# Kernel tuning notes

Measured on AMD Instinct MI355X. Metric: run time of the kernel, lower is better.

## Reference

```python
import jax, jax.numpy as jnp
import numpy as np

N = 24000      # total nodes (8000 per node type)
IN_DIM = 128
OUT_DIM = 128
H = 8          # heads
DK = 16        # out_dim // n_heads
T = 3          # node types (hard-coded in edge_attention)
R = 34         # relations (etypes 0..33 per the etype->ntype rules)
EPR = 10000    # edges per relation (DGL applies edge fn per etype)


def _rel_node_types(num_rel):
    # src/dst node type per relation, transcribed from edge_attention
    src_nt = np.array([0 if r <= 9 else (1 if r <= 21 else 2) for r in range(num_rel)], np.int32)
    def _dnt(r):
        if r <= 2 or 10 <= r <= 13 or 22 <= r <= 24:
            return 0
        if 3 <= r <= 6 or 14 <= r <= 17 or 25 <= r <= 28:
            return 1
        return 2
    dst_nt = np.array([_dnt(r) for r in range(num_rel)], np.int32)
    return src_nt, dst_nt

SRC_NT, DST_NT = _rel_node_types(R)


def setup_inputs() -> dict:
    rng = np.random.default_rng(0)
    Nt = N // T  # nodes of type t live in [t*Nt, (t+1)*Nt)
    src = np.stack([rng.integers(SRC_NT[r] * Nt, (SRC_NT[r] + 1) * Nt, EPR) for r in range(R)]).astype(np.int32)
    dst = np.stack([rng.integers(DST_NT[r] * Nt, (DST_NT[r] + 1) * Nt, EPR) for r in range(R)]).astype(np.int32)
    ks = jax.random.split(jax.random.key(0), 10)
    lin = 1.0 / np.sqrt(IN_DIM)
    return {
        'x': jax.random.normal(ks[0], (N, IN_DIM), jnp.float32),
        'src': jnp.asarray(src),
        'dst': jnp.asarray(dst),
        'Wk': jax.random.normal(ks[1], (T, IN_DIM, OUT_DIM), jnp.float32) * lin,
        'bk': jnp.zeros((T, OUT_DIM), jnp.float32),
        'Wq': jax.random.normal(ks[2], (T, IN_DIM, OUT_DIM), jnp.float32) * lin,
        'bq': jnp.zeros((T, OUT_DIM), jnp.float32),
        'Wv': jax.random.normal(ks[3], (T, IN_DIM, OUT_DIM), jnp.float32) * lin,
        'bv': jnp.zeros((T, OUT_DIM), jnp.float32),
        'Wa': jax.random.normal(ks[4], (T, OUT_DIM, OUT_DIM), jnp.float32) * lin,
        'ba': jnp.zeros((T, OUT_DIM), jnp.float32),
        'rel_att': jax.random.normal(ks[5], (R, H, DK, DK), jnp.float32) / np.sqrt(DK),
        'rel_msg': jax.random.normal(ks[6], (R, H, DK, DK), jnp.float32) / np.sqrt(DK),
        'rel_pri': jnp.ones((R, H), jnp.float32),
        'nta': jnp.ones((T,), jnp.float32),
        'nta1': jnp.ones((T,), jnp.float32),
        'skip': jnp.ones((T,), jnp.float32),
        'weight': jnp.ones((1,), jnp.float32),
        'attn_w': jax.random.normal(ks[7], (2 * DK,), jnp.float32) * 0.1,
    }


def reference(x, src, dst, Wk, bk, Wq, bq, Wv, bv, Wa, ba, rel_att, rel_msg, rel_pri, nta, nta1, skip, weight, attn_w):
    ntype = jnp.repeat(jnp.arange(T), N // T)  # node type per node id
    ridx = jnp.arange(N)

    def typed_lin(h, W, b):
        # per-node-type Linear: compute all T projections, select by node type
        return (jnp.einsum('ni,tio->tno', h, W) + b[:, None, :])[ntype, ridx]

    k = typed_lin(x, Wk, bk).reshape(N, H, DK)
    q = typed_lin(x, Wq, bq).reshape(N, H, DK)
    v = typed_lin(x, Wv, bv).reshape(N, H, DK)

    k_src = k[src]                                   # [R, Epr, H, DK]
    q_dst = q[dst]                                   # [R, Epr, H, DK]
    key_t = jnp.einsum('rehd,rhdf->rehf', k_src, rel_att)
    a = (q_dst * key_t).sum(-1) * rel_pri[:, None, :] / np.sqrt(DK)   # [R, Epr, H]
    val = jnp.einsum('rehd,rhdf->rehf', v[src], rel_msg)              # [R, Epr, H, DK]

    # GAT-style concat attention: attn_fc(cat(att_dst*q, att_src*k)) split into two dots
    wq, wk = attn_w[:DK], attn_w[DK:]
    na = jax.nn.leaky_relu(nta1[DST_NT][:, None, None] * (q_dst @ wq)
                           + nta[SRC_NT][:, None, None] * (k_src @ wk))  # [R, Epr, H]

    beta = jax.nn.sigmoid(weight[0])
    s = (a + beta * na).reshape(R * EPR, H)

    # per-(relation, dst-node) segment softmax (DGL mailbox softmax per etype)
    seg = (jnp.arange(R)[:, None] * N + dst).reshape(-1)
    m = jax.ops.segment_max(s, seg, num_segments=R * N)
    e = jnp.exp(s - m[seg])
    den = jax.ops.segment_sum(e, seg, num_segments=R * N)
    att = e / den[seg]

    vf = val.reshape(R * EPR, H, DK)
    h = jax.ops.segment_sum(att[:, :, None] * vf, seg, num_segments=R * N).reshape(R, N, OUT_DIM)

    # cross_reducer='mean': average over relations that delivered messages to a node
    cnt = jax.ops.segment_sum(jnp.ones((R * EPR,), x.dtype), seg, num_segments=R * N).reshape(R, N)
    nrel = jnp.maximum((cnt > 0).astype(x.dtype).sum(0), 1.0)
    t = h.sum(0) / nrel[:, None]                      # [N, OUT_DIM]

    trans = (jnp.einsum('no,top->tnp', t, Wa) + ba[:, None, :])[ntype, ridx]
    alpha = jax.nn.sigmoid(skip)[ntype][:, None]
    return trans * alpha + x * (1.0 - alpha)
```

## Files before the change

kernel.cpp:

```cpp
#include <hip/hip_runtime.h>

#define NN   24000
#define NTP  8000
#define HH   8
#define DKK  16
#define RR   34
#define EPRN 10000
#define NE   (RR*EPRN)
#define NB   (RR*NTP)
#define CAP  16
#define NSCAT ((NE+255)/256)
#define LOG2E 1.4426950408889634f

typedef short short8 __attribute__((ext_vector_type(8)));
typedef _Float16 half8 __attribute__((ext_vector_type(8)));
typedef float f32x4  __attribute__((ext_vector_type(4)));
typedef _Float16 h2v __attribute__((ext_vector_type(2)));

#if defined(__has_builtin)
# if __has_builtin(__builtin_amdgcn_fdot2)
#  define USE_FDOT2 1
# endif
#endif
#ifndef USE_FDOT2
# define USE_FDOT2 0
#endif

__device__ __forceinline__ int src_nt(int r){ return r<=9?0:(r<=21?1:2); }
__device__ __forceinline__ int dst_nt(int r){
    if (r<=2)  return 0;
    if (r<=6)  return 1;
    if (r<=9)  return 2;
    if (r<=13) return 0;
    if (r<=17) return 1;
    if (r<=21) return 2;
    if (r<=24) return 0;
    if (r<=28) return 1;
    return 2;
}

__device__ __forceinline__ unsigned short bf16rne(float a){
    unsigned int u = __float_as_uint(a);
    u += 0x7fffu + ((u >> 16) & 1u);
    return (unsigned short)(u >> 16);
}
__device__ __forceinline__ unsigned int bf2pack(float a, float b){
    unsigned int ua = __float_as_uint(a);
    unsigned int ub = __float_as_uint(b);
    ua += 0x7fffu + ((ua >> 16) & 1u);
    ub += 0x7fffu + ((ub >> 16) & 1u);
    return (ua >> 16) | (ub & 0xffff0000u);
}
__device__ __forceinline__ unsigned short f16bits(float a){
    _Float16 h = (_Float16)a;
    return __builtin_bit_cast(unsigned short, h);
}

__global__ __launch_bounds__(256) void prep_kernel(
    const float* __restrict__ Wk, const float* __restrict__ Wq,
    const float* __restrict__ Wv, const float* __restrict__ Wa,
    const float* __restrict__ rel_att, const float* __restrict__ rel_msg,
    int* __restrict__ counts, unsigned short* __restrict__ wfrag,
    unsigned short* __restrict__ fragAtt, unsigned short* __restrict__ fragMsg)
{
    const int gid = blockIdx.x * 256 + threadIdx.x;
    if (gid < NB) counts[gid] = 0;
    const int wv   = threadIdx.x >> 6;
    const int lane = threadIdx.x & 63;
    const int m16  = lane & 15, quad = lane >> 4;
    if (blockIdx.x < 96) {
        const int tile = blockIdx.x * 4 + wv;
        const float* W;
        int s, n;
        if (tile < 288) {
            s = tile & 3;
            n = (tile >> 2) & 7;
            const int mat = (tile >> 5) % 3;
            const int tau = tile / 96;
            W = (mat == 0 ? Wk : (mat == 1 ? Wq : Wv)) + (size_t)tau * 16384;
        } else {
            const int t2 = tile - 288;
            s = t2 & 3;
            n = (t2 >> 2) & 7;
            const int tau = t2 >> 5;
            W = Wa + (size_t)tau * 16384;
        }
        const int k0  = s * 32 + quad * 8;
        const int col = n * 16 + m16;
        unsigned short* dstp = wfrag + (size_t)tile * 512 + lane * 8;
        #pragma unroll
        for (int i = 0; i < 8; i++)
            dstp[i] = bf16rne(W[(size_t)(k0 + i) * 128 + col]);
    } else if (blockIdx.x < 164) {
        const int rh = (blockIdx.x - 96) * 4 + wv;
        half8 v;
        #pragma unroll
        for (int i = 0; i < 8; i++) v[i] = (_Float16)0.f;
        if (quad < 2) {
            const float* p = rel_att + ((size_t)rh << 8) + m16 * 16 + quad * 8;
            #pragma unroll
            for (int i = 0; i < 8; i++) v[i] = (_Float16)p[i];
        }
        *(half8*)(fragAtt + ((size_t)rh << 9) + lane * 8) = v;
    } else if (blockIdx.x < 232) {
        const int rh = (blockIdx.x - 164) * 4 + wv;
        half8 v;
        #pragma unroll
        for (int i = 0; i < 8; i++) v[i] = (_Float16)0.f;
        if (quad < 2) {
            const float* Mp = rel_msg + ((size_t)rh << 8);
            #pragma unroll
            for (int i = 0; i < 8; i++) v[i] = (_Float16)Mp[(quad * 8 + i) * 16 + m16];
        }
        *(half8*)(fragMsg + ((size_t)rh << 9) + lane * 8) = v;
    }
}

__global__ __launch_bounds__(256) void work1(
    const float* __restrict__ x,
    const float* __restrict__ bk, const float* __restrict__ bq,
    const float* __restrict__ bv,
    const unsigned short* __restrict__ wfrag,
    const int* __restrict__ src, const int* __restrict__ dst,
    int* __restrict__ counts, int* __restrict__ esrc16,
    float* __restrict__ qo, unsigned short* __restrict__ kvh,
    const float* __restrict__ attn_w,
    float* __restrict__ qwqA, float* __restrict__ kwkA)
{
    __shared__ float qs[4][16][132];
    __shared__ unsigned short ksh[4][16][264];

    if (blockIdx.x >= 375) {
        int e = (blockIdx.x - 375) * 256 + threadIdx.x;
        if (e < NE) {
            int r = e / EPRN;
            int b = r * NTP + (dst[e] - dst_nt(r) * NTP);
            int pos = atomicAdd(&counts[b], 1);
            if (pos < CAP) esrc16[(size_t)b * CAP + pos] = src[e];
        }
        return;
    }

    const int rb   = blockIdx.x * 64;
    const int tau  = rb / NTP;
    const int w    = threadIdx.x >> 6;
    const int lane = threadIdx.x & 63;
    const int m    = lane & 15;
    const int quad = lane >> 4;

    short8 af[4];
    {
        const float* xrow = x + (size_t)(rb + w * 16 + m) * 128;
        #pragma unroll
        for (int s = 0; s < 4; s++) {
            float4 f0 = *(const float4*)(xrow + s * 32 + quad * 8);
            float4 f1 = *(const float4*)(xrow + s * 32 + quad * 8 + 4);
            union { unsigned int u[4]; short8 v; } pk;
            pk.u[0] = bf2pack(f0.x, f0.y); pk.u[1] = bf2pack(f0.z, f0.w);
            pk.u[2] = bf2pack(f1.x, f1.y); pk.u[3] = bf2pack(f1.z, f1.w);
            af[s] = pk.v;
        }
    }

    #pragma unroll
    for (int mat = 0; mat < 3; mat++) {
        const float* bias = (mat == 0 ? bk : (mat == 1 ? bq : bv)) + tau * 128;
        #pragma unroll
        for (int n = 0; n < 8; n++) {
            float bb = bias[n * 16 + m];
            f32x4 acc = {bb, bb, bb, bb};
            #pragma unroll
            for (int s = 0; s < 4; s++) {
                const int tile = ((tau * 3 + mat) * 8 + n) * 4 + s;
                short8 bf = *(const short8*)(wfrag + (size_t)tile * 512 + lane * 8);
                acc = __builtin_amdgcn_mfma_f32_16x16x32_bf16(af[s], bf, acc, 0, 0, 0);
            }
            if (mat == 1) {
                #pragma unroll
                for (int i = 0; i < 4; i++) qs[w][quad * 4 + i][n * 16 + m] = acc[i];
            } else {
                const int off = n * 32 + (mat == 0 ? 0 : 16) + m;
                #pragma unroll
                for (int i = 0; i < 4; i++) ksh[w][quad * 4 + i][off] = f16bits(acc[i]);
            }
        }
        if (mat == 1) {
            __syncthreads();
            #pragma unroll
            for (int j = 0; j < 8; j++) {
                const int id = lane + 64 * j;
                const int row = id >> 5, c4 = id & 31;
                float4 v = *(const float4*)(&qs[w][row][c4 * 4]);
                *(float4*)(qo + (size_t)(rb + w * 16 + row) * 128 + c4 * 4) = v;
            }
        }
    }
    __syncthreads();
    #pragma unroll
    for (int j = 0; j < 8; j++) {
        const int id = lane + 64 * j;
        const int row = id >> 5, c8 = id & 31;
        uint4 u = *(const uint4*)(&ksh[w][row][c8 * 8]);
        *(uint4*)(kvh + (size_t)(rb + w * 16 + row) * 256 + c8 * 8) = u;
    }
    #pragma unroll
    for (int rep = 0; rep < 2; rep++) {
        const int idx = threadIdx.x + rep * 256;
        const int row = idx >> 3, hh = idx & 7;
        const float* qrow = &qs[row >> 4][row & 15][hh * 16];
        const unsigned short* krow = &ksh[row >> 4][row & 15][hh * 32];
        float sq = 0.f, sk = 0.f;
        #pragma unroll
        for (int f = 0; f < 16; f++) {
            sq += qrow[f] * attn_w[f];
            sk += (float)__builtin_bit_cast(_Float16, krow[f]) * attn_w[16 + f];
        }
        qwqA[(size_t)(rb + row) * 8 + hh] = sq;
        kwkA[(size_t)(rb + row) * 8 + hh] = sk;
    }
}

__global__ __launch_bounds__(256) void edge_fused(
    const float* __restrict__ q, const unsigned short* __restrict__ kvh,
    const int* __restrict__ esrc16, const int* __restrict__ counts,
    const unsigned short* __restrict__ fragAtt,
    const unsigned short* __restrict__ fragMsg,
    const float* __restrict__ rel_pri,
    const float* __restrict__ nta, const float* __restrict__ nta1,
    const float* __restrict__ weightp,
    const float* __restrict__ qwqA, const float* __restrict__ kwkA,
    unsigned short* __restrict__ t_bf)
{
    __shared__ float tl[4][64][18];

    const int tid  = threadIdx.x;
    const int w    = tid >> 6;
    const int lane = tid & 63;
    const int h    = __builtin_amdgcn_readfirstlane((tid >> 6) + 4 * blockIdx.y);
    const int base = blockIdx.x * 64;
    const int dn   = base + lane;
    const int dtau = __builtin_amdgcn_readfirstlane(dn / NTP);
    const int dl   = dn - dtau * NTP;
    const int m16  = lane & 15, quad = lane >> 4;

    half8 qf[4];
    #pragma unroll
    for (int g = 0; g < 4; g++) {
        half8 t;
        #pragma unroll
        for (int i = 0; i < 8; i++) t[i] = (_Float16)0.f;
        if (quad < 2) {
            const float* qp = q + (size_t)(base + g * 16 + m16) * 128 + h * 16 + quad * 8;
            #pragma unroll
            for (int i = 0; i < 8; i++) t[i] = (_Float16)qp[i];
        }
        qf[g] = t;
    }

    const float beta = 1.f / (1.f + expf(-weightp[0]));
    const float bl2e = beta * LOG2E;
    const float Pq   = bl2e * nta1[dtau] * qwqA[(size_t)dn * 8 + h];

    f32x4 thacc[4];
    #pragma unroll
    for (int g = 0; g < 4; g++) { f32x4 z = {0.f,0.f,0.f,0.f}; thacc[g] = z; }
    int nrel = 0;

    for (int r = 0; r < RR; r++) {
        if (dst_nt(r) != dtau) continue;
        const int b   = r * NTP + dl;
        int cnt = counts[b];
        cnt = cnt < CAP ? cnt : CAP;
        if (!__any(cnt > 0)) continue;

        half8 Ba = *(const half8*)(fragAtt + (((size_t)r * HH + h) << 9) + lane * 8);
        #pragma unroll
        for (int g = 0; g < 4; g++) {
            f32x4 aq = {0.f, 0.f, 0.f, 0.f};
            aq = __builtin_amdgcn_mfma_f32_16x16x32_f16(qf[g], Ba, aq, 0, 0, 0);
            #pragma unroll
            for (int i = 0; i < 4; i++)
                tl[w][g * 16 + quad * 4 + i][m16] = aq[i];
        }
#if USE_FDOT2
        h2v Aqh[8];
        #pragma unroll
        for (int j = 0; j < 8; j++)
            Aqh[j] = __builtin_bit_cast(h2v,
                __builtin_amdgcn_cvt_pkrtz(tl[w][lane][2*j], tl[w][lane][2*j+1]));
#else
        float Aqf[16];
        #pragma unroll
        for (int d = 0; d < 16; d++) Aqf[d] = tl[w][lane][d];
#endif

        const float pri2 = rel_pri[r * HH + h] * (0.25f * LOG2E);
        const float S    = bl2e * nta[src_nt(r)];
        const int beg = b * CAP;
        int4 e0 = *(const int4*)(esrc16 + beg);
        int4 e1 = *(const int4*)(esrc16 + beg + 4);
        int4 e2 = make_int4(0,0,0,0), e3 = make_int4(0,0,0,0);
        if (__any(cnt > 8)) {
            e2 = *(const int4*)(esrc16 + beg + 8);
            e3 = *(const int4*)(esrc16 + beg + 12);
        }

        float den = 0.f;
        float macc[16] = {};
        #pragma unroll
        for (int ch = 0; ch < 4; ch++) {
            if (!__any(ch * 4 < cnt)) break;
            const int4 cc = (ch == 0) ? e0 : (ch == 1) ? e1 : (ch == 2) ? e2 : e3;
            #pragma unroll
            for (int t = 0; t < 4; t++) {
                const int j = ch * 4 + t;
                if (j < cnt) {
                    const int sn = (t == 0) ? cc.x : (t == 1) ? cc.y : (t == 2) ? cc.z : cc.w;
                    const uint4* kp = (const uint4*)(kvh + (size_t)sn * 256 + h * 32);
                    uint4 u0 = kp[0], u1 = kp[1], u2 = kp[2], u3 = kp[3];
                    const float kwk = kwkA[(size_t)sn * 8 + h];
                    float a = 0.f;
#if USE_FDOT2
                    {
                        const unsigned int kw[8] = {u0.x,u0.y,u0.z,u0.w,u1.x,u1.y,u1.z,u1.w};
                        #pragma unroll
                        for (int i = 0; i < 8; i++)
                            a = __builtin_amdgcn_fdot2(__builtin_bit_cast(h2v, kw[i]), Aqh[i], a, false);
                    }
#else
                    {
                        const unsigned int kw[8] = {u0.x,u0.y,u0.z,u0.w,u1.x,u1.y,u1.z,u1.w};
                        #pragma unroll
                        for (int i = 0; i < 8; i++) {
                            h2v kk2 = __builtin_bit_cast(h2v, kw[i]);
                            a += (float)kk2[0] * Aqf[2*i] + (float)kk2[1] * Aqf[2*i + 1];
                        }
                    }
#endif
                    float vv[16];
                    {
                        const unsigned int vw[8] = {u2.x,u2.y,u2.z,u2.w,u3.x,u3.y,u3.z,u3.w};
                        #pragma unroll
                        for (int i = 0; i < 8; i++) {
                            h2v v2 = __builtin_bit_cast(h2v, vw[i]);
                            vv[2*i] = (float)v2[0]; vv[2*i + 1] = (float)v2[1];
                        }
                    }
                    const float y  = fmaf(S, kwk, Pq);
                    const float na = fmaxf(y, 0.01f * y);
                    const float es = __builtin_amdgcn_exp2f(fmaf(a, pri2, na));
                    den += es;
                    #pragma unroll
                    for (int f = 0; f < 16; f++) macc[f] += es * vv[f];
                }
            }
        }

        float inv = 0.f;
        if (cnt > 0) { inv = 1.0f / den; nrel++; }
        #pragma unroll
        for (int d = 0; d < 16; d++)
            tl[w][lane][d] = macc[d] * inv;

        half8 Bm = *(const half8*)(fragMsg + (((size_t)r * HH + h) << 9) + lane * 8);
        #pragma unroll
        for (int g = 0; g < 4; g++) {
            const float* mp = &tl[w][g * 16 + m16][(quad & 1) * 8];
            half8 am;
            #pragma unroll
            for (int i = 0; i < 8; i++) am[i] = (_Float16)mp[i];
            thacc[g] = __builtin_amdgcn_mfma_f32_16x16x32_f16(am, Bm, thacc[g], 0, 0, 0);
        }
    }

    #pragma unroll
    for (int g = 0; g < 4; g++) {
        #pragma unroll
        for (int i = 0; i < 4; i++)
            tl[w][g * 16 + quad * 4 + i][m16] = thacc[g][i];
    }
    const float innv = 1.f / (float)(nrel > 1 ? nrel : 1);
    float t16[16];
    #pragma unroll
    for (int f = 0; f < 16; f++) t16[f] = tl[w][lane][f] * innv;
    unsigned short* op = t_bf + (size_t)dn * 128 + h * 16;
    uint4 o0, o1;
    o0.x = bf2pack(t16[0],  t16[1]);
    o0.y = bf2pack(t16[2],  t16[3]);
    o0.z = bf2pack(t16[4],  t16[5]);
    o0.w = bf2pack(t16[6],  t16[7]);
    o1.x = bf2pack(t16[8],  t16[9]);
    o1.y = bf2pack(t16[10], t16[11]);
    o1.z = bf2pack(t16[12], t16[13]);
    o1.w = bf2pack(t16[14], t16[15]);
    *(uint4*)(op)     = o0;
    *(uint4*)(op + 8) = o1;
}

__global__ __launch_bounds__(256) void final_mfma(
    const unsigned short* __restrict__ t_bf,
    const unsigned short* __restrict__ wfrag,
    const float* __restrict__ ba, const float* __restrict__ skip,
    const float* __restrict__ x, float* __restrict__ out)
{
    __shared__ float os[4][16][132];
    const int rb   = blockIdx.x * 64;
    const int tau  = rb / NTP;
    const int w    = threadIdx.x >> 6;
    const int lane = threadIdx.x & 63;
    const int m    = lane & 15;
    const int quad = lane >> 4;

    short8 af[4];
    {
        const unsigned short* trow = t_bf + (size_t)(rb + w * 16 + m) * 128;
        #pragma unroll
        for (int s = 0; s < 4; s++)
            af[s] = *(const short8*)(trow + s * 32 + quad * 8);
    }

    #pragma unroll
    for (int n = 0; n < 8; n++) {
        float bb = ba[tau * 128 + n * 16 + m];
        f32x4 acc = {bb, bb, bb, bb};
        #pragma unroll
        for (int s = 0; s < 4; s++) {
            const int tile = 288 + tau * 32 + n * 4 + s;
            short8 bf = *(const short8*)(wfrag + (size_t)tile * 512 + lane * 8);
            acc = __builtin_amdgcn_mfma_f32_16x16x32_bf16(af[s], bf, acc, 0, 0, 0);
        }
        #pragma unroll
        for (int i = 0; i < 4; i++) os[w][quad * 4 + i][n * 16 + m] = acc[i];
    }
    __syncthreads();
    const float alpha = 1.f / (1.f + expf(-skip[tau]));
    const float oma   = 1.f - alpha;
    #pragma unroll
    for (int j = 0; j < 8; j++) {
        const int id = lane + 64 * j;
        const int row = id >> 5, c4 = id & 31;
        float4 t  = *(const float4*)(&os[w][row][c4 * 4]);
        const size_t base = (size_t)(rb + w * 16 + row) * 128 + c4 * 4;
        float4 xv = *(const float4*)(x + base);
        float4 o;
        o.x = t.x * alpha + xv.x * oma;
        o.y = t.y * alpha + xv.y * oma;
        o.z = t.z * alpha + xv.z * oma;
        o.w = t.w * alpha + xv.w * oma;
        *(float4*)(out + base) = o;
    }
}

extern "C" void kernel_launch(void* const* d_in, const int* in_sizes, int n_in,
                              void* d_out, int out_size, void* d_ws, size_t ws_size,
                              hipStream_t stream) {
    const float* x       = (const float*)d_in[0];
    const int*   src     = (const int*)  d_in[1];
    const int*   dst     = (const int*)  d_in[2];
    const float* Wk      = (const float*)d_in[3];
    const float* bk      = (const float*)d_in[4];
    const float* Wq      = (const float*)d_in[5];
    const float* bq      = (const float*)d_in[6];
    const float* Wv      = (const float*)d_in[7];
    const float* bv      = (const float*)d_in[8];
    const float* Wa      = (const float*)d_in[9];
    const float* ba      = (const float*)d_in[10];
    const float* rel_att = (const float*)d_in[11];
    const float* rel_msg = (const float*)d_in[12];
    const float* rel_pri = (const float*)d_in[13];
    const float* nta     = (const float*)d_in[14];
    const float* nta1    = (const float*)d_in[15];
    const float* skip    = (const float*)d_in[16];
    const float* weight  = (const float*)d_in[17];
    const float* attn_w  = (const float*)d_in[18];
    float* out = (float*)d_out;

    float* ws    = (float*)d_ws;
    float* q     = ws;
    unsigned short* kvh = (unsigned short*)(q + (size_t)NN * 128);
    unsigned short* t_bf = kvh + (size_t)NN * 256;
    int* counts  = (int*)(t_bf + (size_t)NN * 128);
    int* esrc16  = counts + NB;
    unsigned short* wfrag = (unsigned short*)(esrc16 + (size_t)NB * CAP);
    unsigned short* fragAtt = wfrag + 384 * 512;
    unsigned short* fragMsg = fragAtt + 272 * 512;
    float* qwqA  = (float*)(fragMsg + 272 * 512);
    float* kwkA  = qwqA + (size_t)NN * 8;

    prep_kernel<<<1063, 256, 0, stream>>>(Wk, Wq, Wv, Wa, rel_att, rel_msg,
                                          counts, wfrag, fragAtt, fragMsg);
    work1<<<375 + NSCAT, 256, 0, stream>>>(x, bk, bq, bv, wfrag,
                                           src, dst, counts, esrc16, q, kvh,
                                           attn_w, qwqA, kwkA);
    edge_fused<<<dim3(NN / 64, 2), 256, 0, stream>>>(
        q, kvh, esrc16, counts, fragAtt, fragMsg, rel_pri,
        nta, nta1, weight, qwqA, kwkA, t_bf);
    final_mfma<<<NN / 64, 256, 0, stream>>>(t_bf, wfrag, ba, skip, x, out);
}
```

Measured before the change: 192.0 us.

## Split edge relations across two grid halves and reduce partials in final kernel

Adds a z dimension to the edge kernel so each destination node's relations are split into two halves. Each half writes bf16 partial sums and a relation count, and final_mfma adds the two halves and divides by the combined count. The kernel body is templated on node type and half, so the relation loop is fully unrolled over compile-time relation lists. This doubles the parallelism of the latency-bound edge kernel, at the cost of extra partial-buffer traffic, a second bf16 rounding, and duplicated q-fragment loads.

Result: no change. 195.0 us (+1.5%).

```diff
diff --git a/kernel.cpp b/kernel.cpp
--- a/kernel.cpp
+++ b/kernel.cpp
@@ -50,6 +50,9 @@
     ua += 0x7fffu + ((ua >> 16) & 1u);
     ub += 0x7fffu + ((ub >> 16) & 1u);
     return (ua >> 16) | (ub & 0xffff0000u);
+}
+__device__ __forceinline__ float bf2f(short v){
+    return __uint_as_float(((unsigned int)(unsigned short)v) << 16);
 }
 __device__ __forceinline__ unsigned short f16bits(float a){
     _Float16 h = (_Float16)a;
@@ -220,7 +223,8 @@
     }
 }
 
-__global__ __launch_bounds__(256) void edge_fused(
+template<int DTAU, int HALF>
+__device__ __forceinline__ void edge_body(
     const float* __restrict__ q, const unsigned short* __restrict__ kvh,
     const int* __restrict__ esrc16, const int* __restrict__ counts,
     const unsigned short* __restrict__ fragAtt,
@@ -229,19 +233,11 @@
     const float* __restrict__ nta, const float* __restrict__ nta1,
     const float* __restrict__ weightp,
     const float* __restrict__ qwqA, const float* __restrict__ kwkA,
-    unsigned short* __restrict__ t_bf)
+    unsigned short* __restrict__ t_part, int* __restrict__ nrelp,
+    float* __restrict__ tlw, int lane, int h, int base, bool writeNrel)
 {
-    __shared__ float tl[4][64][18];
-
-    const int tid  = threadIdx.x;
-    const int w    = tid >> 6;
-    const int lane = tid & 63;
-    const int h    = __builtin_amdgcn_readfirstlane((tid >> 6) + 4 * blockIdx.y);
-    const int base = blockIdx.x * 64;
-    const int dn   = base + lane;
-    const int dtau = __builtin_amdgcn_readfirstlane(dn / NTP);
-    const int dl   = dn - dtau * NTP;
-    const int m16  = lane & 15, quad = lane >> 4;
+    const int dn  = base + lane;
+    const int m16 = lane & 15, quad = lane >> 4;
 
     half8 qf[4];
     #pragma unroll
@@ -259,16 +255,22 @@
 
     const float beta = 1.f / (1.f + expf(-weightp[0]));
     const float bl2e = beta * LOG2E;
-    const float Pq   = bl2e * nta1[dtau] * qwqA[(size_t)dn * 8 + h];
+    const float Pq   = bl2e * nta1[DTAU] * qwqA[(size_t)dn * 8 + h];
 
     f32x4 thacc[4];
     #pragma unroll
     for (int g = 0; g < 4; g++) { f32x4 z = {0.f,0.f,0.f,0.f}; thacc[g] = z; }
     int nrel = 0;
 
-    for (int r = 0; r < RR; r++) {
-        if (dst_nt(r) != dtau) continue;
-        const int b   = r * NTP + dl;
+    constexpr int RCNT = (DTAU == 0) ? 5 : 6;
+    constexpr int RL0[2][6] = {{0,2,11,13,23,-1},{1,10,12,22,24,-1}};
+    constexpr int RL1[2][6] = {{3,5,14,16,25,27},{4,6,15,17,26,28}};
+    constexpr int RL2[2][6] = {{7,9,19,21,30,32},{8,18,20,29,31,33}};
+
+    #pragma unroll
+    for (int ri = 0; ri < RCNT; ri++) {
+        const int r = (DTAU == 0 ? RL0 : (DTAU == 1 ? RL1 : RL2))[HALF][ri];
+        const int b = r * NTP + (dn - DTAU * NTP);
         int cnt = counts[b];
         cnt = cnt < CAP ? cnt : CAP;
         if (!__any(cnt > 0)) continue;
@@ -280,18 +282,18 @@
             aq = __builtin_amdgcn_mfma_f32_16x16x32_f16(qf[g], Ba, aq, 0, 0, 0);
             #pragma unroll
             for (int i = 0; i < 4; i++)
-                tl[w][g * 16 + quad * 4 + i][m16] = aq[i];
+                tlw[(g * 16 + quad * 4 + i) * 19 + m16] = aq[i];
         }
 #if USE_FDOT2
         h2v Aqh[8];
         #pragma unroll
         for (int j = 0; j < 8; j++)
             Aqh[j] = __builtin_bit_cast(h2v,
-                __builtin_amdgcn_cvt_pkrtz(tl[w][lane][2*j], tl[w][lane][2*j+1]));
+                __builtin_amdgcn_cvt_pkrtz(tlw[lane * 19 + 2*j], tlw[lane * 19 + 2*j + 1]));
 #else
         float Aqf[16];
         #pragma unroll
-        for (int d = 0; d < 16; d++) Aqf[d] = tl[w][lane][d];
+        for (int d = 0; d < 16; d++) Aqf[d] = tlw[lane * 19 + d];
 #endif
 
         const float pri2 = rel_pri[r * HH + h] * (0.25f * LOG2E);
@@ -360,12 +362,12 @@
         if (cnt > 0) { inv = 1.0f / den; nrel++; }
         #pragma unroll
         for (int d = 0; d < 16; d++)
-            tl[w][lane][d] = macc[d] * inv;
+            tlw[lane * 19 + d] = macc[d] * inv;
 
         half8 Bm = *(const half8*)(fragMsg + (((size_t)r * HH + h) << 9) + lane * 8);
         #pragma unroll
         for (int g = 0; g < 4; g++) {
-            const float* mp = &tl[w][g * 16 + m16][(quad & 1) * 8];
+            const float* mp = &tlw[(g * 16 + m16) * 19 + (quad & 1) * 8];
             half8 am;
             #pragma unroll
             for (int i = 0; i < 8; i++) am[i] = (_Float16)mp[i];
@@ -377,13 +379,12 @@
     for (int g = 0; g < 4; g++) {
         #pragma unroll
         for (int i = 0; i < 4; i++)
-            tl[w][g * 16 + quad * 4 + i][m16] = thacc[g][i];
-    }
-    const float innv = 1.f / (float)(nrel > 1 ? nrel : 1);
+            tlw[(g * 16 + quad * 4 + i) * 19 + m16] = thacc[g][i];
+    }
     float t16[16];
     #pragma unroll
-    for (int f = 0; f < 16; f++) t16[f] = tl[w][lane][f] * innv;
-    unsigned short* op = t_bf + (size_t)dn * 128 + h * 16;
+    for (int f = 0; f < 16; f++) t16[f] = tlw[lane * 19 + f];
+    unsigned short* op = t_part + ((size_t)(HALF * NN + dn)) * 128 + h * 16;
     uint4 o0, o1;
     o0.x = bf2pack(t16[0],  t16[1]);
     o0.y = bf2pack(t16[2],  t16[3]);
@@ -395,10 +396,56 @@
     o1.w = bf2pack(t16[14], t16[15]);
     *(uint4*)(op)     = o0;
     *(uint4*)(op + 8) = o1;
+    if (writeNrel) nrelp[HALF * NN + dn] = nrel;
+}
+
+__global__ __launch_bounds__(256) void edge_fused(
+    const float* __restrict__ q, const unsigned short* __restrict__ kvh,
+    const int* __restrict__ esrc16, const int* __restrict__ counts,
+    const unsigned short* __restrict__ fragAtt,
+    const unsigned short* __restrict__ fragMsg,
+    const float* __restrict__ rel_pri,
+    const float* __restrict__ nta, const float* __restrict__ nta1,
+    const float* __restrict__ weightp,
+    const float* __restrict__ qwqA, const float* __restrict__ kwkA,
+    unsigned short* __restrict__ t_part, int* __restrict__ nrelp)
+{
+    __shared__ float tl[4][64][19];
+
+    const int tid  = threadIdx.x;
+    const int w    = tid >> 6;
+    const int lane = tid & 63;
+    const int h    = __builtin_amdgcn_readfirstlane((tid >> 6) + 4 * blockIdx.y);
+    const int base = blockIdx.x * 64;
+    float* tlw = &tl[w][0][0];
+    const bool wn = (blockIdx.y == 0) && (w == 0);
+
+    if (blockIdx.x < 125) {
+        if (blockIdx.z == 0)
+            edge_body<0,0>(q,kvh,esrc16,counts,fragAtt,fragMsg,rel_pri,nta,nta1,
+                           weightp,qwqA,kwkA,t_part,nrelp,tlw,lane,h,base,wn);
+        else
+            edge_body<0,1>(q,kvh,esrc16,counts,fragAtt,fragMsg,rel_pri,nta,nta1,
+                           weightp,qwqA,kwkA,t_part,nrelp,tlw,lane,h,base,wn);
+    } else if (blockIdx.x < 250) {
+        if (blockIdx.z == 0)
+            edge_body<1,0>(q,kvh,esrc16,counts,fragAtt,fragMsg,rel_pri,nta,nta1,
+                           weightp,qwqA,kwkA,t_part,nrelp,tlw,lane,h,base,wn);
+        else
+            edge_body<1,1>(q,kvh,esrc16,counts,fragAtt,fragMsg,rel_pri,nta,nta1,
+                           weightp,qwqA,kwkA,t_part,nrelp,tlw,lane,h,base,wn);
+    } else {
+        if (blockIdx.z == 0)
+            edge_body<2,0>(q,kvh,esrc16,counts,fragAtt,fragMsg,rel_pri,nta,nta1,
+                           weightp,qwqA,kwkA,t_part,nrelp,tlw,lane,h,base,wn);
+        else
+            edge_body<2,1>(q,kvh,esrc16,counts,fragAtt,fragMsg,rel_pri,nta,nta1,
+                           weightp,qwqA,kwkA,t_part,nrelp,tlw,lane,h,base,wn);
+    }
 }
 
 __global__ __launch_bounds__(256) void final_mfma(
-    const unsigned short* __restrict__ t_bf,
+    const unsigned short* __restrict__ t_part, const int* __restrict__ nrelp,
     const unsigned short* __restrict__ wfrag,
     const float* __restrict__ ba, const float* __restrict__ skip,
     const float* __restrict__ x, float* __restrict__ out)
@@ -411,12 +458,27 @@
     const int m    = lane & 15;
     const int quad = lane >> 4;
 
+    const int row = rb + w * 16 + m;
+    const int nr  = nrelp[row] + nrelp[NN + row];
+    const float innv = 1.f / (float)(nr > 1 ? nr : 1);
+
     short8 af[4];
     {
-        const unsigned short* trow = t_bf + (size_t)(rb + w * 16 + m) * 128;
-        #pragma unroll
-        for (int s = 0; s < 4; s++)
-            af[s] = *(const short8*)(trow + s * 32 + quad * 8);
+        const unsigned short* t0 = t_part + (size_t)row * 128;
+        const unsigned short* t1 = t_part + (size_t)(NN + row) * 128;
+        #pragma unroll
+        for (int s = 0; s < 4; s++) {
+            short8 a0 = *(const short8*)(t0 + s * 32 + quad * 8);
+            short8 a1 = *(const short8*)(t1 + s * 32 + quad * 8);
+            union { unsigned int u[4]; short8 v; } pk;
+            #pragma unroll
+            for (int p = 0; p < 4; p++) {
+                float fa = (bf2f(a0[2*p])   + bf2f(a1[2*p]))   * innv;
+                float fb = (bf2f(a0[2*p+1]) + bf2f(a1[2*p+1])) * innv;
+                pk.u[p] = bf2pack(fa, fb);
+            }
+            af[s] = pk.v;
+        }
     }
 
     #pragma unroll
@@ -438,9 +500,9 @@
     #pragma unroll
     for (int j = 0; j < 8; j++) {
         const int id = lane + 64 * j;
-        const int row = id >> 5, c4 = id & 31;
-        float4 t  = *(const float4*)(&os[w][row][c4 * 4]);
-        const size_t base = (size_t)(rb + w * 16 + row) * 128 + c4 * 4;
+        const int r2 = id >> 5, c4 = id & 31;
+        float4 t  = *(const float4*)(&os[w][r2][c4 * 4]);
+        const size_t base = (size_t)(rb + w * 16 + r2) * 128 + c4 * 4;
         float4 xv = *(const float4*)(x + base);
         float4 o;
         o.x = t.x * alpha + xv.x * oma;
@@ -478,8 +540,9 @@
     float* ws    = (float*)d_ws;
     float* q     = ws;
     unsigned short* kvh = (unsigned short*)(q + (size_t)NN * 128);
-    unsigned short* t_bf = kvh + (size_t)NN * 256;
-    int* counts  = (int*)(t_bf + (size_t)NN * 128);
+    unsigned short* t_part = kvh + (size_t)NN * 256;
+    int* nrelp   = (int*)(t_part + (size_t)2 * NN * 128);
+    int* counts  = nrelp + 2 * NN;
     int* esrc16  = counts + NB;
     unsigned short* wfrag = (unsigned short*)(esrc16 + (size_t)NB * CAP);
     unsigned short* fragAtt = wfrag + 384 * 512;
@@ -492,8 +555,8 @@
     work1<<<375 + NSCAT, 256, 0, stream>>>(x, bk, bq, bv, wfrag,
                                            src, dst, counts, esrc16, q, kvh,
                                            attn_w, qwqA, kwkA);
-    edge_fused<<<dim3(NN / 64, 2), 256, 0, stream>>>(
+    edge_fused<<<dim3(375, 2, 2), 256, 0, stream>>>(
         q, kvh, esrc16, counts, fragAtt, fragMsg, rel_pri,
-        nta, nta1, weight, qwqA, kwkA, t_bf);
-    final_mfma<<<NN / 64, 256, 0, stream>>>(t_bf, wfrag, ba, skip, x, out);
-}
+        nta, nta1, weight, qwqA, kwkA, t_part, nrelp);
+    final_mfma<<<NN / 64, 256, 0, stream>>>(t_part, nrelp, wfrag, ba, skip, x, out);
+}
```
